# Optimization experiments

Hardware: AMD Instinct MI355X
Metric: run time of the kernel (lower is better)

Reference implementation:

```python
import jax, jax.numpy as jnp
import numpy as np

C_IN = 1024
N_TILES = 64
C_OUT = 512
BN = 32768  # b * n_tiles, b = 512


def setup_inputs() -> dict:
    key = jax.random.key(0)
    ks = jax.random.split(key, 7)
    s = 1.0 / np.sqrt(C_IN)
    x = jax.random.normal(ks[0], (BN, C_IN), dtype=jnp.float32)
    # torch nn.Linear params: weight (c_out, c_in), bias (c_out,)
    Wk = jax.random.uniform(ks[1], (C_OUT, C_IN), jnp.float32, -s, s)
    bk = jax.random.uniform(ks[2], (C_OUT,), jnp.float32, -s, s)
    Wq = jax.random.uniform(ks[3], (C_OUT, C_IN), jnp.float32, -s, s)
    bq = jax.random.uniform(ks[4], (C_OUT,), jnp.float32, -s, s)
    Wv = jax.random.uniform(ks[5], (C_OUT, C_IN), jnp.float32, -s, s)
    bv = jax.random.uniform(ks[6], (C_OUT,), jnp.float32, -s, s)
    return {"x": x, "Wk": Wk, "bk": bk, "Wq": Wq, "bq": bq, "Wv": Wv, "bv": bv}


def reference(x, Wk, bk, Wq, bq, Wv, bv):
    bn, c = x.shape
    b = bn // N_TILES
    # QKV projections (torch Linear: x @ W.T + b)
    keys = (x @ Wk.T + bk).reshape(b, N_TILES, C_OUT)
    queries = (x @ Wq.T + bq).reshape(b, N_TILES, C_OUT)
    values = (x @ Wv.T + bv).reshape(b, N_TILES, C_OUT)
    # attention_weights[b, t, s] = sum_c keys[b,t,c] * queries[b,s,c]  -> (b, n_tiles, n_tiles)
    aw = jnp.einsum('btc,bsc->bts', keys, queries)
    # NOTE: softmax is over the BATCH axis (dim=0), as in the original module
    aw = jax.nn.softmax(aw / jnp.sqrt(jnp.float32(C_OUT)), axis=0)
    # out[b, c, s] = sum_t values[b,t,c] * aw[b,t,s]  -> (b, c_out, n_tiles)
    out = jnp.einsum('btc,bts->bcs', values, aw)
    return out
```

## Files before the change

kernel.cpp:

```cpp
#include <hip/hip_runtime.h>
#include <hip/hip_bf16.h>


typedef __bf16 bf16;
using i32x4 = __attribute__((ext_vector_type(4))) int;

#define NT     64
#define BATCH  512

#define OFF_XQH 0ul
#define OFF_XQL 33554432ul
#define OFF_WT  67108864ul
#define OFF_K   70254592ul
#define OFF_Q   103809024ul
#define OFF_V   137363456ul
#define OFF_AW  204472320ul
#define OFF_MS  212860928ul

__global__ void quant_all(const float* __restrict__ x,
                          unsigned int* __restrict__ qh,
                          unsigned int* __restrict__ ql, float invXS,
                          const float* __restrict__ W0,
                          const float* __restrict__ W1,
                          const float* __restrict__ W2,
                          char* __restrict__ WT, float invWS) {
  if (blockIdx.x < 2048) {
    int i = blockIdx.x * 256 + threadIdx.x;
    for (; i < 8388608; i += 2048 * 256) {
      float4 v = ((const float4*)x)[i];
      unsigned hw = 0, lw = 0;
#pragma unroll
      for (int j = 0; j < 4; ++j) {
        float f = (j == 0) ? v.x : (j == 1) ? v.y : (j == 2) ? v.z : v.w;
        int q = __float2int_rn(f * invXS);
        q = max(-16320, min(16319, q));
        int h = (q + 64) >> 7;
        int lo = q - (h << 7);
        hw |= ((unsigned)(h & 0xFF)) << (8 * j);
        lw |= ((unsigned)(lo & 0xFF)) << (8 * j);
      }
      qh[i] = hw;
      ql[i] = lw;
    }
  } else {
    int gid = (blockIdx.x - 2048) * 256 + threadIdx.x;
    int proj = gid >> 17;
    int idx = gid & 131071;
    const float* W = (proj == 0) ? W0 : (proj == 1 ? W1 : W2);
    int c = idx >> 8, k = (idx & 255) * 4;
    float4 v = ((const float4*)W)[idx];
    unsigned hw = 0, lw = 0;
#pragma unroll
    for (int j = 0; j < 4; ++j) {
      float f = (j == 0) ? v.x : (j == 1) ? v.y : (j == 2) ? v.z : v.w;
      int q = __float2int_rn(f * invWS);
      q = max(-16320, min(16319, q));
      int h = (q + 64) >> 7;
      int lo = q - (h << 7);
      hw |= ((unsigned)(h & 0xFF)) << (8 * j);
      lw |= ((unsigned)(lo & 0xFF)) << (8 * j);
    }
    int kc = k >> 6, kg = (k >> 4) & 3, ki = k & 15;
    int ct = c >> 4, lane = (c & 15) | (kg << 4);
    size_t dst = (size_t)proj * 1048576 + (size_t)(ct * 16 + kc) * 2048 +
                 lane * 16 + ki;
    *(unsigned int*)(WT + dst) = hw;
    *(unsigned int*)(WT + dst + 1024) = lw;
  }
}

__device__ __forceinline__ void gl16(const char* g, char* l) {
  __builtin_amdgcn_global_load_lds(
      (const __attribute__((address_space(1))) unsigned int*)g,
      (__attribute__((address_space(3))) unsigned int*)l, 16, 0, 0);
}

#define VMC(n)  asm volatile("s_waitcnt vmcnt(" #n ")" ::: "memory")
#define LGKM0   asm volatile("s_waitcnt lgkmcnt(0)" ::: "memory")
#define BAR     __builtin_amdgcn_s_barrier()
#define SGB     __builtin_amdgcn_sched_barrier(0)
#define MFMA8   __builtin_amdgcn_mfma_i32_16x16x64_i8

__global__ __launch_bounds__(512, 2) void gemm_i8(
    const char* __restrict__ XQH, const char* __restrict__ XQL,
    const char* __restrict__ WT,
    const float* __restrict__ bk, const float* __restrict__ bq,
    const float* __restrict__ bv,
    bf16* __restrict__ K, bf16* __restrict__ Q, float* __restrict__ V) {
  __shared__ __align__(16) char lds[131072];

  const int bid = (blockIdx.x & 7) * 96 + (blockIdx.x >> 3);
  const int mt = bid / 6, nb = bid % 6;
  const int gm0 = mt * 256;
  const int proj = nb >> 1;
  const int nbl = nb & 1;
  const int wn0 = nbl * 256;

  const int tid = threadIdx.x;
  const int l = tid & 63, w = tid >> 6;
  const int wr = w >> 2, wc = w & 3;
  const int lr = l & 15, lk = l >> 4;

  const char* aqh0 = XQH + (size_t)(gm0 + ((tid >> 6) << 4) + (tid & 15)) * 1024
                         + (((tid >> 4) & 3) << 4);
  const char* aql0 = XQL + (size_t)(gm0 + ((tid >> 6) << 4) + (tid & 15)) * 1024
                         + (((tid >> 4) & 3) << 4);
  const char* wph0 = WT + (size_t)proj * 1048576 +
                     (size_t)(nbl * 16 + (tid >> 6)) * 32768 + (tid & 63) * 16;
  const char* wpl0 = wph0 + 1024;
  const int dT = tid * 16;

  const int rdA = (wr * 8) * 1024 + l * 16;
  const int rdB = 32768 + (wc * 4) * 1024 + l * 16;

  i32x4 acc[8][4] = {};
  const i32x4 Z = {0, 0, 0, 0};

  auto stAqh = [&](int kc, int bo) {
    const int kA = kc * 64;
    gl16(aqh0 + kA, lds + bo + dT);
    gl16(aqh0 + 131072 + kA, lds + bo + 8192 + dT);
  };
  auto stAql = [&](int kc, int bo) {
    const int kA = kc * 64;
    gl16(aql0 + kA, lds + bo + 16384 + dT);
    gl16(aql0 + 131072 + kA, lds + bo + 24576 + dT);
  };
  auto stBph = [&](int kc, int bo) {
    const int kB = kc * 2048;
    gl16(wph0 + kB, lds + bo + 32768 + dT);
    gl16(wph0 + 262144 + kB, lds + bo + 40960 + dT);
  };
  auto stBpl = [&](int kc, int bo) {
    const int kB = kc * 2048;
    gl16(wpl0 + kB, lds + bo + 49152 + dT);
    gl16(wpl0 + 262144 + kB, lds + bo + 57344 + dT);
  };

  stAqh(0, 0); stBpl(0, 0); stBph(0, 0); stAql(0, 0);
  VMC(4);
  BAR;

  auto chunk = [&](int kc, bool last) {
    const int bo = (kc & 1) * 65536, nbuf = bo ^ 65536;
    i32x4 aHa[4], aHb[4], aLa[4], aLb[4], bH[4], bL[4];

#pragma unroll
    for (int m = 0; m < 4; ++m)
      aHa[m] = *(const i32x4*)(lds + bo + rdA + m * 1024);
#pragma unroll
    for (int n = 0; n < 4; ++n)
      bL[n] = *(const i32x4*)(lds + bo + rdB + 16384 + n * 1024);
    if (!last) stAqh(kc + 1, nbuf);
    BAR; LGKM0; SGB;
    __builtin_amdgcn_s_setprio(1);
#pragma unroll
    for (int m = 0; m < 4; ++m)
#pragma unroll
      for (int n = 0; n < 4; ++n)
        acc[m][n] = MFMA8(aHa[m], bL[n], acc[m][n], 0, 0, 0);
    __builtin_amdgcn_s_setprio(0);
    BAR;

#pragma unroll
    for (int m = 0; m < 4; ++m)
      aHb[m] = *(const i32x4*)(lds + bo + rdA + (m + 4) * 1024);
    if (!last) { stBpl(kc + 1, nbuf); VMC(6); } else { VMC(2); }
    BAR; LGKM0; SGB;
    __builtin_amdgcn_s_setprio(1);
#pragma unroll
    for (int m = 0; m < 4; ++m)
#pragma unroll
      for (int n = 0; n < 4; ++n)
        acc[m + 4][n] = MFMA8(aHb[m], bL[n], acc[m + 4][n], 0, 0, 0);
    __builtin_amdgcn_s_setprio(0);
    BAR;

#pragma unroll
    for (int n = 0; n < 4; ++n)
      bH[n] = *(const i32x4*)(lds + bo + rdB + n * 1024);
    if (!last) { stBph(kc + 1, nbuf); VMC(6); } else { VMC(0); }
    BAR; LGKM0; SGB;
    __builtin_amdgcn_s_setprio(1);
#pragma unroll
    for (int n = 0; n < 4; ++n) {
      i32x4 t0 = MFMA8(aHb[0], bH[n], Z, 0, 0, 0);
      i32x4 t1 = MFMA8(aHb[1], bH[n], Z, 0, 0, 0);
      i32x4 t2 = MFMA8(aHb[2], bH[n], Z, 0, 0, 0);
      i32x4 t3 = MFMA8(aHb[3], bH[n], Z, 0, 0, 0);
      acc[4][n] = acc[4][n] + (t0 << 7);
      acc[5][n] = acc[5][n] + (t1 << 7);
      acc[6][n] = acc[6][n] + (t2 << 7);
      acc[7][n] = acc[7][n] + (t3 << 7);
    }
    __builtin_amdgcn_s_setprio(0);
    BAR;

#pragma unroll
    for (int m = 0; m < 4; ++m)
      aLa[m] = *(const i32x4*)(lds + bo + 16384 + rdA + m * 1024);
    if (!last) stAql(kc + 1, nbuf);
    BAR; LGKM0; SGB;
    __builtin_amdgcn_s_setprio(1);
#pragma unroll
    for (int n = 0; n < 4; ++n) {
      i32x4 t0 = MFMA8(aHa[0], bH[n], Z, 0, 0, 0);
      i32x4 t1 = MFMA8(aHa[1], bH[n], Z, 0, 0, 0);
      i32x4 t2 = MFMA8(aHa[2], bH[n], Z, 0, 0, 0);
      i32x4 t3 = MFMA8(aHa[3], bH[n], Z, 0, 0, 0);
      acc[0][n] = acc[0][n] + (t0 << 7);
      acc[1][n] = acc[1][n] + (t1 << 7);
      acc[2][n] = acc[2][n] + (t2 << 7);
      acc[3][n] = acc[3][n] + (t3 << 7);
    }
    __builtin_amdgcn_s_setprio(0);
    BAR;

#pragma unroll
    for (int m = 0; m < 4; ++m)
      aLb[m] = *(const i32x4*)(lds + bo + 16384 + rdA + (m + 4) * 1024);
    if (!last) VMC(4);
    BAR; LGKM0; SGB;
    __builtin_amdgcn_s_setprio(1);
#pragma unroll
    for (int m = 0; m < 4; ++m)
#pragma unroll
      for (int n = 0; n < 4; ++n)
        acc[m][n] = MFMA8(aLa[m], bH[n], acc[m][n], 0, 0, 0);
    __builtin_amdgcn_s_setprio(0);
    BAR;

    __builtin_amdgcn_s_setprio(1);
#pragma unroll
    for (int m = 0; m < 4; ++m)
#pragma unroll
      for (int n = 0; n < 4; ++n)
        acc[m + 4][n] = MFMA8(aLb[m], bH[n], acc[m + 4][n], 0, 0, 0);
    __builtin_amdgcn_s_setprio(0);
  };

  for (int kc = 0; kc < 15; ++kc) chunk(kc, false);
  chunk(15, true);

  const float SCC = 128.0f * (6.0f / 16256.0f) * (0.03125f / 16320.0f);
  const float* bias = (proj == 0) ? bk : (proj == 1 ? bq : bv);
  if (proj == 2) {
#pragma unroll
    for (int m = 0; m < 8; ++m) {
      const int row0 = gm0 + wr * 128 + m * 16 + lk * 4;
#pragma unroll
      for (int n = 0; n < 4; ++n) {
        const int col = wn0 + wc * 64 + n * 16 + lr;
        const float bb = bias[col];
#pragma unroll
        for (int r = 0; r < 4; ++r)
          V[(size_t)(row0 + r) * 512 + col] =
              SCC * (float)acc[m][n][r] + bb;
      }
    }
  } else {
    bf16* Ob = (proj == 0) ? K : Q;
#pragma unroll
    for (int m = 0; m < 8; ++m) {
      const int row0 = gm0 + wr * 128 + m * 16 + lk * 4;
#pragma unroll
      for (int n = 0; n < 4; ++n) {
        const int col = wn0 + wc * 64 + n * 16 + lr;
        const float bb = bias[col];
#pragma unroll
        for (int r = 0; r < 4; ++r)
          Ob[(size_t)(row0 + r) * 512 + col] =
              (bf16)(SCC * (float)acc[m][n][r] + bb);
      }
    }
  }
}

__global__ __launch_bounds__(256) void logits_kernel(
    const bf16* __restrict__ K, const bf16* __restrict__ Q,
    float* __restrict__ E) {
  __shared__ float Ks[64][68];
  __shared__ float Qs[64][68];
  const int b = blockIdx.x;
  const unsigned short* Kb = (const unsigned short*)(K + (size_t)b * 32768);
  const unsigned short* Qb = (const unsigned short*)(Q + (size_t)b * 32768);
  const int tid = threadIdx.x;
  const int tr = tid >> 4, tc = tid & 15;
  const int srow = tid >> 2;
  const int scb = (tid & 3) * 16;

  float acc[4][4] = {};
  for (int c0 = 0; c0 < 512; c0 += 64) {
    __syncthreads();
    {
      const unsigned short* kp = Kb + srow * 512 + c0 + scb;
      const unsigned short* qp = Qb + srow * 512 + c0 + scb;
      uint4 k0 = *(const uint4*)kp, k1 = *(const uint4*)(kp + 8);
      uint4 q0 = *(const uint4*)qp, q1 = *(const uint4*)(qp + 8);
      unsigned ku[8] = {k0.x, k0.y, k0.z, k0.w, k1.x, k1.y, k1.z, k1.w};
      unsigned qu[8] = {q0.x, q0.y, q0.z, q0.w, q1.x, q1.y, q1.z, q1.w};
#pragma unroll
      for (int j = 0; j < 8; ++j) {
        Ks[scb + 2 * j][srow]     = __uint_as_float(ku[j] << 16);
        Ks[scb + 2 * j + 1][srow] = __uint_as_float(ku[j] & 0xffff0000u);
        Qs[scb + 2 * j][srow]     = __uint_as_float(qu[j] << 16);
        Qs[scb + 2 * j + 1][srow] = __uint_as_float(qu[j] & 0xffff0000u);
      }
    }
    __syncthreads();
#pragma unroll 4
    for (int cc = 0; cc < 64; ++cc) {
      float4 kx = *(const float4*)&Ks[cc][tr * 4];
      float4 qx = *(const float4*)&Qs[cc][tc * 4];
#pragma unroll
      for (int i = 0; i < 4; ++i)
#pragma unroll
        for (int j = 0; j < 4; ++j) acc[i][j] += kx[i] * qx[j];
    }
  }
  const float scale = 0.04419417382415922f;
#pragma unroll
  for (int i = 0; i < 4; ++i)
#pragma unroll
    for (int j = 0; j < 4; ++j)
      E[(size_t)b * 4096 + (tr * 4 + i) * 64 + (tc * 4 + j)] =
          __expf(acc[i][j] * scale);
}

__global__ __launch_bounds__(1024) void sums_kernel(
    const float* __restrict__ E, float* __restrict__ I) {
  __shared__ float red[16][64];
  const int tt = blockIdx.x;
  const int tid = threadIdx.x;
  const int s = tid & 63, bq = tid >> 6;
  const size_t base = (size_t)tt * 64 + s;

  float sum = 0.f;
  for (int b = bq * 32; b < bq * 32 + 32; ++b)
    sum += E[(size_t)b * 4096 + base];
  red[bq][s] = sum;
  __syncthreads();
  if (bq == 0) {
    float total = 0.f;
#pragma unroll
    for (int i = 0; i < 16; ++i) total += red[i][s];
    I[tt * 64 + s] = 1.0f / total;
  }
}

__global__ __launch_bounds__(1024) void out_kernel(
    const float* __restrict__ V, const float* __restrict__ E,
    const float* __restrict__ I, float* __restrict__ out) {
  __shared__ float Vs[32768];
  __shared__ float Ps[64][64];
  const int b = blockIdx.x;
  const int tid = threadIdx.x;
  const float* Vb = V + (size_t)b * 32768;
  const float* Eb = E + (size_t)b * 4096;

#pragma unroll
  for (int j = 0; j < 8; ++j) {
    int u = j * 1024 + tid;
    ((float4*)Vs)[u] = ((const float4*)Vb)[u];
  }
  for (int i = tid; i < 4096; i += 1024)
    Ps[i >> 6][i & 63] = Eb[i] * I[i];
  __syncthreads();

  const int s = tid & 63, cw = tid >> 6;
  const int c0 = cw * 32;
  float a[32] = {};
  for (int t = 0; t < 64; ++t) {
    float p = Ps[t][s];
    const float4* vr = (const float4*)(Vs + t * 512 + c0);
#pragma unroll
    for (int j = 0; j < 8; ++j) {
      float4 v = vr[j];
      a[4 * j + 0] += v.x * p;
      a[4 * j + 1] += v.y * p;
      a[4 * j + 2] += v.z * p;
      a[4 * j + 3] += v.w * p;
    }
  }
  float* Ob = out + (size_t)b * 32768;
#pragma unroll
  for (int j = 0; j < 32; ++j)
    Ob[(size_t)(c0 + j) * 64 + s] = a[j];
}

extern "C" void kernel_launch(void* const* d_in, const int* in_sizes, int n_in,
                              void* d_out, int out_size, void* d_ws,
                              size_t ws_size, hipStream_t stream) {
  const float* x  = (const float*)d_in[0];
  const float* Wk = (const float*)d_in[1];
  const float* bk = (const float*)d_in[2];
  const float* Wq = (const float*)d_in[3];
  const float* bq = (const float*)d_in[4];
  const float* Wv = (const float*)d_in[5];
  const float* bv = (const float*)d_in[6];
  float* out = (float*)d_out;

  char* ws = (char*)d_ws;
  unsigned int* XQH = (unsigned int*)(ws + OFF_XQH);
  unsigned int* XQL = (unsigned int*)(ws + OFF_XQL);
  char* WT = ws + OFF_WT;
  bf16* K  = (bf16*)(ws + OFF_K);
  bf16* Q  = (bf16*)(ws + OFF_Q);
  float* V  = (float*)(ws + OFF_V);
  float* E  = (float*)(ws + OFF_AW);
  float* I  = (float*)(ws + OFF_MS);

  const float invXS = 16256.0f / 6.0f;
  const float invWS = 16320.0f / 0.03125f;

  quant_all<<<3584, 256, 0, stream>>>(x, XQH, XQL, invXS, Wk, Wq, Wv, WT,
                                      invWS);

  gemm_i8<<<768, 512, 0, stream>>>((const char*)XQH, (const char*)XQL,
                                   WT, bk, bq, bv, K, Q, V);

  logits_kernel<<<BATCH, 256, 0, stream>>>(K, Q, E);
  sums_kernel<<<NT, 1024, 0, stream>>>(E, I);
  out_kernel<<<BATCH, 1024, 0, stream>>>(V, E, I, out);
}
```

Before: 273.2 us.

## Use bf16 MFMA for attention logits and drop explicit LDS waits in GEMM

```diff
diff --git a/kernel.cpp b/kernel.cpp
--- a/kernel.cpp
+++ b/kernel.cpp
@@ -3,7 +3,9 @@
 
 
 typedef __bf16 bf16;
-using i32x4 = __attribute__((ext_vector_type(4))) int;
+using i32x4  = __attribute__((ext_vector_type(4))) int;
+using bf16x8 = __attribute__((ext_vector_type(8))) __bf16;
+using f32x4  = __attribute__((ext_vector_type(4))) float;
 
 #define NT     64
 #define BATCH  512
@@ -76,9 +78,7 @@
 }
 
 #define VMC(n)  asm volatile("s_waitcnt vmcnt(" #n ")" ::: "memory")
-#define LGKM0   asm volatile("s_waitcnt lgkmcnt(0)" ::: "memory")
 #define BAR     __builtin_amdgcn_s_barrier()
-#define SGB     __builtin_amdgcn_sched_barrier(0)
 #define MFMA8   __builtin_amdgcn_mfma_i32_16x16x64_i8
 
 __global__ __launch_bounds__(512, 2) void gemm_i8(
@@ -152,7 +152,7 @@
     for (int n = 0; n < 4; ++n)
       bL[n] = *(const i32x4*)(lds + bo + rdB + 16384 + n * 1024);
     if (!last) stAqh(kc + 1, nbuf);
-    BAR; LGKM0; SGB;
+    BAR;
     __builtin_amdgcn_s_setprio(1);
 #pragma unroll
     for (int m = 0; m < 4; ++m)
@@ -166,7 +166,7 @@
     for (int m = 0; m < 4; ++m)
       aHb[m] = *(const i32x4*)(lds + bo + rdA + (m + 4) * 1024);
     if (!last) { stBpl(kc + 1, nbuf); VMC(6); } else { VMC(2); }
-    BAR; LGKM0; SGB;
+    BAR;
     __builtin_amdgcn_s_setprio(1);
 #pragma unroll
     for (int m = 0; m < 4; ++m)
@@ -180,7 +180,7 @@
     for (int n = 0; n < 4; ++n)
       bH[n] = *(const i32x4*)(lds + bo + rdB + n * 1024);
     if (!last) { stBph(kc + 1, nbuf); VMC(6); } else { VMC(0); }
-    BAR; LGKM0; SGB;
+    BAR;
     __builtin_amdgcn_s_setprio(1);
 #pragma unroll
     for (int n = 0; n < 4; ++n) {
@@ -200,7 +200,7 @@
     for (int m = 0; m < 4; ++m)
       aLa[m] = *(const i32x4*)(lds + bo + 16384 + rdA + m * 1024);
     if (!last) stAql(kc + 1, nbuf);
-    BAR; LGKM0; SGB;
+    BAR;
     __builtin_amdgcn_s_setprio(1);
 #pragma unroll
     for (int n = 0; n < 4; ++n) {
@@ -220,7 +220,7 @@
     for (int m = 0; m < 4; ++m)
       aLb[m] = *(const i32x4*)(lds + bo + 16384 + rdA + (m + 4) * 1024);
     if (!last) VMC(4);
-    BAR; LGKM0; SGB;
+    BAR;
     __builtin_amdgcn_s_setprio(1);
 #pragma unroll
     for (int m = 0; m < 4; ++m)
@@ -279,52 +279,43 @@
 __global__ __launch_bounds__(256) void logits_kernel(
     const bf16* __restrict__ K, const bf16* __restrict__ Q,
     float* __restrict__ E) {
-  __shared__ float Ks[64][68];
-  __shared__ float Qs[64][68];
+  __shared__ __align__(16) char lds[131072];
   const int b = blockIdx.x;
-  const unsigned short* Kb = (const unsigned short*)(K + (size_t)b * 32768);
-  const unsigned short* Qb = (const unsigned short*)(Q + (size_t)b * 32768);
   const int tid = threadIdx.x;
-  const int tr = tid >> 4, tc = tid & 15;
-  const int srow = tid >> 2;
-  const int scb = (tid & 3) * 16;
-
-  float acc[4][4] = {};
-  for (int c0 = 0; c0 < 512; c0 += 64) {
-    __syncthreads();
-    {
-      const unsigned short* kp = Kb + srow * 512 + c0 + scb;
-      const unsigned short* qp = Qb + srow * 512 + c0 + scb;
-      uint4 k0 = *(const uint4*)kp, k1 = *(const uint4*)(kp + 8);
-      uint4 q0 = *(const uint4*)qp, q1 = *(const uint4*)(qp + 8);
-      unsigned ku[8] = {k0.x, k0.y, k0.z, k0.w, k1.x, k1.y, k1.z, k1.w};
-      unsigned qu[8] = {q0.x, q0.y, q0.z, q0.w, q1.x, q1.y, q1.z, q1.w};
-#pragma unroll
-      for (int j = 0; j < 8; ++j) {
-        Ks[scb + 2 * j][srow]     = __uint_as_float(ku[j] << 16);
-        Ks[scb + 2 * j + 1][srow] = __uint_as_float(ku[j] & 0xffff0000u);
-        Qs[scb + 2 * j][srow]     = __uint_as_float(qu[j] << 16);
-        Qs[scb + 2 * j + 1][srow] = __uint_as_float(qu[j] & 0xffff0000u);
-      }
-    }
-    __syncthreads();
-#pragma unroll 4
-    for (int cc = 0; cc < 64; ++cc) {
-      float4 kx = *(const float4*)&Ks[cc][tr * 4];
-      float4 qx = *(const float4*)&Qs[cc][tc * 4];
-#pragma unroll
-      for (int i = 0; i < 4; ++i)
-#pragma unroll
-        for (int j = 0; j < 4; ++j) acc[i][j] += kx[i] * qx[j];
-    }
-  }
+  const int l = tid & 63, w = tid >> 6;
+
+  const char* Kb = (const char*)(K + (size_t)b * 32768);
+  const char* Qb = (const char*)(Q + (size_t)b * 32768);
+  const size_t so = (size_t)((tid >> 6) * 16 + (l & 15)) * 1024 +
+                    ((l >> 4) * 8) * 2;
+  const int dT = tid * 16;
+#pragma unroll
+  for (int j = 0; j < 16; ++j) {
+    gl16(Kb + so + j * 64, lds + j * 4096 + dT);
+    gl16(Qb + so + j * 64, lds + 65536 + j * 4096 + dT);
+  }
+  VMC(0);
+  BAR;
+
+  f32x4 acc[4] = {};
+  for (int ks = 0; ks < 16; ++ks) {
+    bf16x8 bF = *(const bf16x8*)(lds + 65536 + (ks * 4 + w) * 1024 + l * 16);
+#pragma unroll
+    for (int m = 0; m < 4; ++m) {
+      bf16x8 aF = *(const bf16x8*)(lds + (ks * 4 + m) * 1024 + l * 16);
+      acc[m] = __builtin_amdgcn_mfma_f32_16x16x32_bf16(aF, bF, acc[m], 0, 0, 0);
+    }
+  }
+
   const float scale = 0.04419417382415922f;
-#pragma unroll
-  for (int i = 0; i < 4; ++i)
-#pragma unroll
-    for (int j = 0; j < 4; ++j)
-      E[(size_t)b * 4096 + (tr * 4 + i) * 64 + (tc * 4 + j)] =
-          __expf(acc[i][j] * scale);
+  float* Eb = E + (size_t)b * 4096;
+  const int s = w * 16 + (l & 15);
+  const int r0 = (l >> 4) * 4;
+#pragma unroll
+  for (int m = 0; m < 4; ++m)
+#pragma unroll
+    for (int r = 0; r < 4; ++r)
+      Eb[(m * 16 + r0 + r) * 64 + s] = __expf(acc[m][r] * scale);
 }
 
 __global__ __launch_bounds__(1024) void sums_kernel(
```

New measurement: 253.0 us. 1.08x faster.
